# Performance work log

Hardware: AMD Instinct MI355X
Metric: run time of the kernel (lower is better)

The kernel has to match this reference:

```python
import jax, jax.numpy as jnp
import numpy as np

B, S, H = 8, 2048, 1024

def setup_inputs() -> dict:
    key = jax.random.key(0)
    k1, k2 = jax.random.split(key)
    inputs = jax.random.normal(k1, (B, S, H), dtype=jnp.float32)
    # PyTorch Linear weight [out, in]; init ~ U(-1/sqrt(H), 1/sqrt(H)) approximated with scaled normal
    W = jax.random.normal(k2, (H, H), dtype=jnp.float32) * (1.0 / np.sqrt(H))
    b = jnp.zeros((H,), dtype=jnp.float32)
    return {"inputs": inputs, "W": W, "b": b}

def reference(inputs, W, b):
    # QW = inputs @ W^T + b   (nn.Linear)
    QW = jnp.einsum('bsh,oh->bso', inputs, W) + b  # [B,S,H]
    # score = QW @ inputs^T  (no scaling, no mask)
    score = jnp.einsum('bqh,bkh->bqk', QW, inputs)  # [B,S,S]
    attn = jax.nn.softmax(score, axis=2)
    # output = attn @ inputs
    output = jnp.einsum('bqk,bkh->bqh', attn, inputs)  # [B,S,H]
    return output
```

## Files before the change

### kernel.cpp

```cpp
#include <hip/hip_runtime.h>
#include <hip/hip_bf16.h>
#include <hip/hip_fp16.h>

typedef unsigned short u16;
typedef __attribute__((ext_vector_type(8))) _Float16 f16x8;
typedef __attribute__((ext_vector_type(4))) float f32x4;

#define B_ 8
#define S_ 2048
#define H_ 1024
#define M_ (B_ * S_)

__device__ __forceinline__ u16 f2h(float f) {
  _Float16 h = (_Float16)f;
  return __builtin_bit_cast(u16, h);
}

__global__ void f32_to_f16_kernel(const float* __restrict__ x,
                                  u16* __restrict__ o, int n4) {
  int stride = gridDim.x * blockDim.x;
  for (int i = blockIdx.x * blockDim.x + threadIdx.x; i < n4; i += stride) {
    float4 v = reinterpret_cast<const float4*>(x)[i];
    ushort4 h;
    h.x = f2h(v.x); h.y = f2h(v.y); h.z = f2h(v.z); h.w = f2h(v.w);
    reinterpret_cast<ushort4*>(o)[i] = h;
  }
}

__global__ __launch_bounds__(256) void transpose_f32_kernel(
    const float* __restrict__ x, u16* __restrict__ xt, u16* __restrict__ xf) {
  __shared__ u16 t[64][72];
  int b = blockIdx.z, s0 = blockIdx.x * 64, h0 = blockIdx.y * 64;
  int tid = threadIdx.x;
  int row = tid & 63, seg = tid >> 6;
  const float* src = x + ((size_t)(b * S_ + s0 + row)) * H_ + h0 + seg * 16;
  u16* dstf = xf + ((size_t)(b * S_ + s0 + row)) * H_ + h0 + seg * 16;
#pragma unroll
  for (int j = 0; j < 4; ++j) {
    float4 v = reinterpret_cast<const float4*>(src)[j];
    ushort4 h;
    h.x = f2h(v.x); h.y = f2h(v.y); h.z = f2h(v.z); h.w = f2h(v.w);
    reinterpret_cast<ushort4*>(dstf)[j] = h;
    *reinterpret_cast<ushort4*>(&t[row][seg * 16 + j * 4]) = h;
  }
  __syncthreads();
  int hh = tid & 63, ss = tid >> 6;
  u16* dst = xt + ((size_t)(b * H_ + h0 + hh)) * S_ + s0 + ss * 16;
#pragma unroll
  for (int j = 0; j < 4; ++j) {
    ushort4 o;
    o.x = t[ss * 16 + j * 4 + 0][hh];
    o.y = t[ss * 16 + j * 4 + 1][hh];
    o.z = t[ss * 16 + j * 4 + 2][hh];
    o.w = t[ss * 16 + j * 4 + 3][hh];
    reinterpret_cast<ushort4*>(dst)[j] = o;
  }
}

__device__ __forceinline__ void async_stage16(const u16* g, u16* l) {
  __builtin_amdgcn_global_load_lds(
      (__attribute__((address_space(1))) void*)g,
      (__attribute__((address_space(3))) void*)l, 16, 0, 0);
}

template <int OM>
__global__ __launch_bounds__(512) void gemm8_kernel(
    const u16* __restrict__ A, const u16* __restrict__ B,
    float* __restrict__ Cf, u16* __restrict__ Ch,
    const float* __restrict__ bias,
    int lda, int ldb, int ldc, int K,
    long sAz, long sBz, long sCz) {
  __shared__ __align__(16) u16 sA[2][256 * 64];
  __shared__ __align__(16) u16 sB[2][256 * 64];

  int gx = gridDim.x, gy = gridDim.y;
  int nwg = gx * gy * gridDim.z;
  int wgid = blockIdx.x + gx * (blockIdx.y + gy * blockIdx.z);
  int q = nwg >> 3, r = nwg & 7;
  int xcd = wgid & 7, idx = wgid >> 3;
  int nid = (xcd < r ? xcd * (q + 1) : r * (q + 1) + (xcd - r) * q) + idx;
  int bxi = nid % gx, t2 = nid / gx;
  int byi = t2 % gy, bzi = t2 / gy;

  int tid = threadIdx.x, wave = tid >> 6, lane = tid & 63;
  int wm = wave >> 2, wn = wave & 3;
  int bm = bxi * 256, bn = byi * 256;
  long zA = (long)bzi * sAz;
  long zB = (long)bzi * sBz;
  long zC = (long)bzi * sCz;
  const u16* gA = A + zA + (size_t)bm * lda;
  const u16* gB = B + zB + (size_t)bn * ldb;

  int srow = tid >> 3;
  int scolb = (tid & 7) << 4;
  int sco = (scolb ^ ((srow & 7) << 4)) >> 1;
  size_t aO0 = (size_t)srow * lda + sco, aO1 = aO0 + (size_t)64 * lda;
  size_t bO0 = (size_t)srow * ldb + sco, bO1 = bO0 + (size_t)64 * ldb;
  int ld0 = srow * 64 + (scolb >> 1), ld1 = ld0 + 64 * 64;

  auto stgA = [&](int slot, int half, int kofs) {
    const u16* g = gA + (size_t)(half * 128) * lda + kofs;
    u16* l = &sA[slot][half * 8192];
    async_stage16(g + aO0, l + ld0);
    async_stage16(g + aO1, l + ld1);
  };
  auto stgB = [&](int slot, int half, int kofs) {
    const u16* g = gB + (size_t)(half * 128) * ldb + kofs;
    u16* l = &sB[slot][half * 8192];
    async_stage16(g + bO0, l + ld0);
    async_stage16(g + bO1, l + ld1);
  };

  int la = lane & 15;
  int kg = (lane >> 4) << 4;
  auto frag = [&](const u16* base, int row, int colb) -> f16x8 {
    int off = (row << 7) + (colb ^ ((row & 7) << 4));
    return *reinterpret_cast<const f16x8*>(
        reinterpret_cast<const char*>(base) + off);
  };

  f16x8 aF[4][2];
  f16x8 bF[2][2][2];
  f32x4 acc[8][4] = {};

  auto RA = [&](int slot, int qm) {
#pragma unroll
    for (int j = 0; j < 4; ++j)
#pragma unroll
      for (int ks = 0; ks < 2; ++ks)
        aF[j][ks] = frag(sA[slot], qm * 128 + (j * 2 + wm) * 16 + la,
                         ks * 64 + kg);
  };
  auto RB = [&](int slot, int qn) {
#pragma unroll
    for (int i = 0; i < 2; ++i)
#pragma unroll
      for (int ks = 0; ks < 2; ++ks)
        bF[qn][i][ks] = frag(sB[slot], qn * 128 + (i * 4 + wn) * 16 + la,
                             ks * 64 + kg);
  };
  auto MM = [&](int qm, int qn) {
#pragma unroll
    for (int ks = 0; ks < 2; ++ks)
#pragma unroll
      for (int j = 0; j < 4; ++j)
#pragma unroll
        for (int i = 0; i < 2; ++i)
          acc[qm * 4 + j][qn * 2 + i] = __builtin_amdgcn_mfma_f32_16x16x32_f16(
              aF[j][ks], bF[qn][i][ks], acc[qm * 4 + j][qn * 2 + i], 0, 0, 0);
  };

#define VM6 asm volatile("s_waitcnt vmcnt(6)" ::: "memory")
#define VM0 asm volatile("s_waitcnt vmcnt(0)" ::: "memory")
#define BAR __builtin_amdgcn_s_barrier()
#define LG0                                              \
  asm volatile("s_waitcnt lgkmcnt(0)" ::: "memory");     \
  __builtin_amdgcn_sched_barrier(0)
#define MFMA_CL(qm, qn)                 \
  __builtin_amdgcn_s_setprio(1);        \
  MM(qm, qn);                           \
  __builtin_amdgcn_s_setprio(0)

  int NT = K >> 6;
  stgA(0, 0, 0); stgB(0, 0, 0); stgB(0, 1, 0); stgA(0, 1, 0);
  if (NT > 1) { stgA(1, 0, 64); stgB(1, 1, 64); stgA(1, 1, 64); }
  VM6;
  BAR;

  for (int t = 0; t < NT; ++t) {
    int s = t & 1, ns = s ^ 1;
    int k1 = (t + 1) << 6, k2 = (t + 2) << 6;
    bool p1 = (t + 1 < NT), p2 = (t + 2 < NT);
    RA(s, 0); RB(s, 0);
    if (p1) stgB(ns, 0, k1);
    LG0; MFMA_CL(0, 0); BAR;
    RB(s, 1);
    if (p2) stgA(s, 0, k2);
    LG0; MFMA_CL(0, 1); BAR;
    RA(s, 1);
    if (p2) stgB(s, 1, k2);
    LG0; MFMA_CL(1, 1); BAR;
    if (p2) stgA(s, 1, k2);
    MFMA_CL(1, 0);
    if (t < NT - 2) { VM6; } else if (t == NT - 2) { VM0; }
    BAR;
  }
#undef VM6
#undef VM0
#undef BAR
#undef LG0
#undef MFMA_CL

#pragma unroll
  for (int mf = 0; mf < 8; ++mf) {
    int qm = mf >> 2, j = mf & 3;
    int row = bm + qm * 128 + (j * 2 + wm) * 16 + (lane >> 4) * 4;
#pragma unroll
    for (int nf = 0; nf < 4; ++nf) {
      int qn = nf >> 1, i = nf & 1;
      int col = bn + qn * 128 + (i * 4 + wn) * 16 + la;
#pragma unroll
      for (int r = 0; r < 4; ++r) {
        float v = acc[mf][nf][r];
        if constexpr (OM == 1) {
          Ch[zC + (size_t)(row + r) * ldc + col] = f2h(v + bias[col]);
        } else {
          Cf[zC + (size_t)(row + r) * ldc + col] = v;
        }
      }
    }
  }
}

__global__ __launch_bounds__(256) void softmax_kernel(const float* __restrict__ sc,
                                                      u16* __restrict__ attn,
                                                      int opitch) {
  __shared__ float red[4];
  size_t row = blockIdx.x;
  const float* p = sc + row * S_;
  u16* o = attn + row * (size_t)opitch;
  int t = threadIdx.x;
  float4 v0 = reinterpret_cast<const float4*>(p)[t];
  float4 v1 = reinterpret_cast<const float4*>(p)[t + 256];
  float mx = fmaxf(fmaxf(fmaxf(v0.x, v0.y), fmaxf(v0.z, v0.w)),
                   fmaxf(fmaxf(v1.x, v1.y), fmaxf(v1.z, v1.w)));
#pragma unroll
  for (int d = 32; d > 0; d >>= 1) mx = fmaxf(mx, __shfl_xor(mx, d));
  if ((t & 63) == 0) red[t >> 6] = mx;
  __syncthreads();
  mx = fmaxf(fmaxf(red[0], red[1]), fmaxf(red[2], red[3]));
  float e[8];
  e[0] = __expf(v0.x - mx); e[1] = __expf(v0.y - mx);
  e[2] = __expf(v0.z - mx); e[3] = __expf(v0.w - mx);
  e[4] = __expf(v1.x - mx); e[5] = __expf(v1.y - mx);
  e[6] = __expf(v1.z - mx); e[7] = __expf(v1.w - mx);
  float s = ((e[0] + e[1]) + (e[2] + e[3])) + ((e[4] + e[5]) + (e[6] + e[7]));
#pragma unroll
  for (int d = 32; d > 0; d >>= 1) s += __shfl_xor(s, d);
  __syncthreads();
  if ((t & 63) == 0) red[t >> 6] = s;
  __syncthreads();
  s = (red[0] + red[1]) + (red[2] + red[3]);
  float inv = 1.0f / s;
  ushort4 h0, h1;
  h0.x = f2h(e[0] * inv); h0.y = f2h(e[1] * inv);
  h0.z = f2h(e[2] * inv); h0.w = f2h(e[3] * inv);
  h1.x = f2h(e[4] * inv); h1.y = f2h(e[5] * inv);
  h1.z = f2h(e[6] * inv); h1.w = f2h(e[7] * inv);
  reinterpret_cast<ushort4*>(o)[t] = h0;
  reinterpret_cast<ushort4*>(o)[t + 256] = h1;
}

extern "C" void kernel_launch(void* const* d_in, const int* in_sizes, int n_in,
                              void* d_out, int out_size, void* d_ws, size_t ws_size,
                              hipStream_t stream) {
  const float* X = (const float*)d_in[0];
  const float* W = (const float*)d_in[1];
  const float* bias = (const float*)d_in[2];
  float* out = (float*)d_out;
  char* ws = (char*)d_ws;

  const size_t MB = 1ull << 20;
  u16* XF = (u16*)(ws);
  u16* WF = (u16*)(ws + 32 * MB);
  u16* XT = (u16*)(ws + 34 * MB);
  u16* QW = (u16*)(ws + 66 * MB);
  float* SC = (float*)(ws + 98 * MB);
  u16* PF = (u16*)(ws + 162 * MB);

  int plan = (ws_size >= 226 * MB) ? 2 : (ws_size >= 163 * MB) ? 1 : 0;
  int CB = (plan >= 1) ? 4 : 2;
  int nch = B_ / CB;

  f32_to_f16_kernel<<<1024, 256, 0, stream>>>(W, WF, H_ * H_ / 4);
  transpose_f32_kernel<<<dim3(S_ / 64, H_ / 64, B_), 256, 0, stream>>>(
      X, XT, XF);
  gemm8_kernel<1><<<dim3(M_ / 256, H_ / 256, 1), 512, 0, stream>>>(
      XF, WF, nullptr, QW, bias, H_, H_, H_, H_, 0, 0, 0);
  for (int ch = 0; ch < nch; ++ch) {
    long off = (long)ch * CB;
    gemm8_kernel<0><<<dim3(S_ / 256, S_ / 256, CB), 512, 0, stream>>>(
        QW + off * S_ * H_, XF + off * S_ * H_, SC, nullptr, nullptr,
        H_, H_, S_, H_, (long)S_ * H_, (long)S_ * H_, (long)S_ * S_);
    if (plan == 2) {
      softmax_kernel<<<CB * S_, 256, 0, stream>>>(
          SC, PF + off * S_ * S_, S_);
    } else {
      softmax_kernel<<<CB * S_, 256, 0, stream>>>(
          SC, (u16*)SC, 2 * S_);
      gemm8_kernel<0><<<dim3(S_ / 256, H_ / 256, CB), 512, 0, stream>>>(
          (u16*)SC, XT + off * (long)H_ * S_,
          out + off * (long)S_ * H_, nullptr, nullptr,
          2 * S_, S_, H_, S_, (long)S_ * 2 * S_, (long)H_ * S_, (long)S_ * H_);
    }
  }
  if (plan == 2) {
    gemm8_kernel<0><<<dim3(S_ / 256, H_ / 256, B_), 512, 0, stream>>>(
        PF, XT, out, nullptr, nullptr,
        S_, S_, H_, S_, (long)S_ * S_, (long)H_ * S_, (long)S_ * H_);
  }
}
```

Measured before the change: 263.7 us.

## Switch GEMM to 32x32x16 MFMA and always softmax in place

Replaces the 16x16x32 MFMA tiling with 32x32x16 MFMA instructions. Each wave now holds 4x2 accumulator tiles of 16 floats, with fragment loads and the epilogue row mapping rewritten to match. The host plan no longer writes fp16 probabilities to a separate buffer; softmax writes in place into the score buffer, and with enough workspace all 8 batches run as one chunk. The larger MFMA shape cuts LDS fragment reads per FLOP, while the scattered epilogue stores and larger chunk's scratch footprint may change memory behaviour.

Measured after the change: 274.5 us. +4.1%, slower.

```diff
diff --git a/kernel.cpp b/kernel.cpp
--- a/kernel.cpp
+++ b/kernel.cpp
@@ -4,7 +4,7 @@
 
 typedef unsigned short u16;
 typedef __attribute__((ext_vector_type(8))) _Float16 f16x8;
-typedef __attribute__((ext_vector_type(4))) float f32x4;
+typedef __attribute__((ext_vector_type(16))) float f32x16;
 
 #define B_ 8
 #define S_ 2048
@@ -111,43 +111,38 @@
     async_stage16(g + bO1, l + ld1);
   };
 
-  int la = lane & 15;
-  int kg = (lane >> 4) << 4;
+  int l31 = lane & 31;
+  int kg32 = (lane >> 5) << 4;
   auto frag = [&](const u16* base, int row, int colb) -> f16x8 {
     int off = (row << 7) + (colb ^ ((row & 7) << 4));
     return *reinterpret_cast<const f16x8*>(
         reinterpret_cast<const char*>(base) + off);
   };
 
-  f16x8 aF[4][2];
-  f16x8 bF[2][2][2];
-  f32x4 acc[8][4] = {};
+  f16x8 aF[2][4];
+  f16x8 bF[2][4];
+  f32x16 acc[4][2] = {};
 
   auto RA = [&](int slot, int qm) {
 #pragma unroll
-    for (int j = 0; j < 4; ++j)
-#pragma unroll
-      for (int ks = 0; ks < 2; ++ks)
-        aF[j][ks] = frag(sA[slot], qm * 128 + (j * 2 + wm) * 16 + la,
-                         ks * 64 + kg);
+    for (int mt = 0; mt < 2; ++mt)
+#pragma unroll
+      for (int ks = 0; ks < 4; ++ks)
+        aF[mt][ks] = frag(sA[slot], qm * 128 + wm * 64 + mt * 32 + l31,
+                          ks * 32 + kg32);
   };
   auto RB = [&](int slot, int qn) {
 #pragma unroll
-    for (int i = 0; i < 2; ++i)
-#pragma unroll
-      for (int ks = 0; ks < 2; ++ks)
-        bF[qn][i][ks] = frag(sB[slot], qn * 128 + (i * 4 + wn) * 16 + la,
-                             ks * 64 + kg);
+    for (int ks = 0; ks < 4; ++ks)
+      bF[qn][ks] = frag(sB[slot], qn * 128 + wn * 32 + l31, ks * 32 + kg32);
   };
   auto MM = [&](int qm, int qn) {
 #pragma unroll
-    for (int ks = 0; ks < 2; ++ks)
-#pragma unroll
-      for (int j = 0; j < 4; ++j)
-#pragma unroll
-        for (int i = 0; i < 2; ++i)
-          acc[qm * 4 + j][qn * 2 + i] = __builtin_amdgcn_mfma_f32_16x16x32_f16(
-              aF[j][ks], bF[qn][i][ks], acc[qm * 4 + j][qn * 2 + i], 0, 0, 0);
+    for (int ks = 0; ks < 4; ++ks)
+#pragma unroll
+      for (int mt = 0; mt < 2; ++mt)
+        acc[qm * 2 + mt][qn] = __builtin_amdgcn_mfma_f32_32x32x16_f16(
+            aF[mt][ks], bF[qn][ks], acc[qm * 2 + mt][qn], 0, 0, 0);
   };
 
 #define VM6 asm volatile("s_waitcnt vmcnt(6)" ::: "memory")
@@ -191,21 +186,22 @@
 #undef LG0
 #undef MFMA_CL
 
-#pragma unroll
-  for (int mf = 0; mf < 8; ++mf) {
-    int qm = mf >> 2, j = mf & 3;
-    int row = bm + qm * 128 + (j * 2 + wm) * 16 + (lane >> 4) * 4;
-#pragma unroll
-    for (int nf = 0; nf < 4; ++nf) {
-      int qn = nf >> 1, i = nf & 1;
-      int col = bn + qn * 128 + (i * 4 + wn) * 16 + la;
-#pragma unroll
-      for (int r = 0; r < 4; ++r) {
-        float v = acc[mf][nf][r];
+  int rsub = 4 * (lane >> 5);
+#pragma unroll
+  for (int mi = 0; mi < 4; ++mi) {
+    int qm = mi >> 1, mt = mi & 1;
+    int rowb = bm + qm * 128 + wm * 64 + mt * 32 + rsub;
+#pragma unroll
+    for (int ni = 0; ni < 2; ++ni) {
+      int col = bn + ni * 128 + wn * 32 + l31;
+#pragma unroll
+      for (int reg = 0; reg < 16; ++reg) {
+        int row = rowb + (reg & 3) + 8 * (reg >> 2);
+        float v = acc[mi][ni][reg];
         if constexpr (OM == 1) {
-          Ch[zC + (size_t)(row + r) * ldc + col] = f2h(v + bias[col]);
+          Ch[zC + (size_t)row * ldc + col] = f2h(v + bias[col]);
         } else {
-          Cf[zC + (size_t)(row + r) * ldc + col] = v;
+          Cf[zC + (size_t)row * ldc + col] = v;
         }
       }
     }
@@ -266,10 +262,8 @@
   u16* XT = (u16*)(ws + 34 * MB);
   u16* QW = (u16*)(ws + 66 * MB);
   float* SC = (float*)(ws + 98 * MB);
-  u16* PF = (u16*)(ws + 162 * MB);
-
-  int plan = (ws_size >= 226 * MB) ? 2 : (ws_size >= 163 * MB) ? 1 : 0;
-  int CB = (plan >= 1) ? 4 : 2;
+
+  int CB = (ws_size >= 226 * MB) ? 8 : 4;
   int nch = B_ / CB;
 
   f32_to_f16_kernel<<<1024, 256, 0, stream>>>(W, WF, H_ * H_ / 4);
@@ -282,21 +276,10 @@
     gemm8_kernel<0><<<dim3(S_ / 256, S_ / 256, CB), 512, 0, stream>>>(
         QW + off * S_ * H_, XF + off * S_ * H_, SC, nullptr, nullptr,
         H_, H_, S_, H_, (long)S_ * H_, (long)S_ * H_, (long)S_ * S_);
-    if (plan == 2) {
-      softmax_kernel<<<CB * S_, 256, 0, stream>>>(
-          SC, PF + off * S_ * S_, S_);
-    } else {
-      softmax_kernel<<<CB * S_, 256, 0, stream>>>(
-          SC, (u16*)SC, 2 * S_);
-      gemm8_kernel<0><<<dim3(S_ / 256, H_ / 256, CB), 512, 0, stream>>>(
-          (u16*)SC, XT + off * (long)H_ * S_,
-          out + off * (long)S_ * H_, nullptr, nullptr,
-          2 * S_, S_, H_, S_, (long)S_ * 2 * S_, (long)H_ * S_, (long)S_ * H_);
-    }
-  }
-  if (plan == 2) {
-    gemm8_kernel<0><<<dim3(S_ / 256, H_ / 256, B_), 512, 0, stream>>>(
-        PF, XT, out, nullptr, nullptr,
-        S_, S_, H_, S_, (long)S_ * S_, (long)H_ * S_, (long)S_ * H_);
-  }
-}
+    softmax_kernel<<<CB * S_, 256, 0, stream>>>(SC, (u16*)SC, 2 * S_);
+    gemm8_kernel<0><<<dim3(S_ / 256, H_ / 256, CB), 512, 0, stream>>>(
+        (u16*)SC, XT + off * (long)H_ * S_,
+        out + off * (long)S_ * H_, nullptr, nullptr,
+        2 * S_, S_, H_, S_, (long)S_ * 2 * S_, (long)H_ * S_, (long)S_ * H_);
+  }
+}
```

## Double-buffer MFMA fragments in GEMM and batch full attention chunks in place

Applied to the files above, without the earlier changes.

The GEMM inner loop now keeps separate register sets for the two A and two B quadrant fragments. It loads B for both quadrants up front and loads A1 while the first MFMA clusters run. The explicit lgkmcnt(0) waits and sched_barriers are dropped so LDS reads can overlap with MFMAs, at the cost of more VGPR pressure and relying on the compiler to insert the needed waits. The host plan also drops the separate PF probability buffer. It processes all 8 batches in one chunk (or 4 with less workspace), with softmax written in place and the P·V GEMM run per chunk.

New measurement: 257.5 us. -2.3%, faster.

```diff
diff --git a/kernel.cpp b/kernel.cpp
--- a/kernel.cpp
+++ b/kernel.cpp
@@ -119,27 +119,27 @@
         reinterpret_cast<const char*>(base) + off);
   };
 
-  f16x8 aF[4][2];
-  f16x8 bF[2][2][2];
+  f16x8 aF0[4][2], aF1[4][2];
+  f16x8 bF0[2][2], bF1[2][2];
   f32x4 acc[8][4] = {};
 
-  auto RA = [&](int slot, int qm) {
+  auto RA = [&](int slot, int qm, f16x8(&dst)[4][2]) {
 #pragma unroll
     for (int j = 0; j < 4; ++j)
 #pragma unroll
       for (int ks = 0; ks < 2; ++ks)
-        aF[j][ks] = frag(sA[slot], qm * 128 + (j * 2 + wm) * 16 + la,
-                         ks * 64 + kg);
-  };
-  auto RB = [&](int slot, int qn) {
+        dst[j][ks] = frag(sA[slot], qm * 128 + (j * 2 + wm) * 16 + la,
+                          ks * 64 + kg);
+  };
+  auto RB = [&](int slot, int qn, f16x8(&dst)[2][2]) {
 #pragma unroll
     for (int i = 0; i < 2; ++i)
 #pragma unroll
       for (int ks = 0; ks < 2; ++ks)
-        bF[qn][i][ks] = frag(sB[slot], qn * 128 + (i * 4 + wn) * 16 + la,
-                             ks * 64 + kg);
-  };
-  auto MM = [&](int qm, int qn) {
+        dst[i][ks] = frag(sB[slot], qn * 128 + (i * 4 + wn) * 16 + la,
+                          ks * 64 + kg);
+  };
+  auto MM = [&](int qm, int qn, f16x8(&a)[4][2], f16x8(&b)[2][2]) {
 #pragma unroll
     for (int ks = 0; ks < 2; ++ks)
 #pragma unroll
@@ -147,19 +147,14 @@
 #pragma unroll
         for (int i = 0; i < 2; ++i)
           acc[qm * 4 + j][qn * 2 + i] = __builtin_amdgcn_mfma_f32_16x16x32_f16(
-              aF[j][ks], bF[qn][i][ks], acc[qm * 4 + j][qn * 2 + i], 0, 0, 0);
+              a[j][ks], b[i][ks], acc[qm * 4 + j][qn * 2 + i], 0, 0, 0);
   };
 
 #define VM6 asm volatile("s_waitcnt vmcnt(6)" ::: "memory")
 #define VM0 asm volatile("s_waitcnt vmcnt(0)" ::: "memory")
 #define BAR __builtin_amdgcn_s_barrier()
-#define LG0                                              \
-  asm volatile("s_waitcnt lgkmcnt(0)" ::: "memory");     \
-  __builtin_amdgcn_sched_barrier(0)
-#define MFMA_CL(qm, qn)                 \
-  __builtin_amdgcn_s_setprio(1);        \
-  MM(qm, qn);                           \
-  __builtin_amdgcn_s_setprio(0)
+#define PRIO1 __builtin_amdgcn_s_setprio(1)
+#define PRIO0 __builtin_amdgcn_s_setprio(0)
 
   int NT = K >> 6;
   stgA(0, 0, 0); stgB(0, 0, 0); stgB(0, 1, 0); stgA(0, 1, 0);
@@ -171,25 +166,25 @@
     int s = t & 1, ns = s ^ 1;
     int k1 = (t + 1) << 6, k2 = (t + 2) << 6;
     bool p1 = (t + 1 < NT), p2 = (t + 2 < NT);
-    RA(s, 0); RB(s, 0);
+    RA(s, 0, aF0); RB(s, 0, bF0);
+    RB(s, 1, bF1);
     if (p1) stgB(ns, 0, k1);
-    LG0; MFMA_CL(0, 0); BAR;
-    RB(s, 1);
+    PRIO1; MM(0, 0, aF0, bF0); PRIO0; BAR;
+    RA(s, 1, aF1);
     if (p2) stgA(s, 0, k2);
-    LG0; MFMA_CL(0, 1); BAR;
-    RA(s, 1);
+    PRIO1; MM(0, 1, aF0, bF1); PRIO0; BAR;
     if (p2) stgB(s, 1, k2);
-    LG0; MFMA_CL(1, 1); BAR;
+    PRIO1; MM(1, 1, aF1, bF1); PRIO0; BAR;
     if (p2) stgA(s, 1, k2);
-    MFMA_CL(1, 0);
+    PRIO1; MM(1, 0, aF1, bF0); PRIO0;
     if (t < NT - 2) { VM6; } else if (t == NT - 2) { VM0; }
     BAR;
   }
 #undef VM6
 #undef VM0
 #undef BAR
-#undef LG0
-#undef MFMA_CL
+#undef PRIO1
+#undef PRIO0
 
 #pragma unroll
   for (int mf = 0; mf < 8; ++mf) {
@@ -266,10 +261,8 @@
   u16* XT = (u16*)(ws + 34 * MB);
   u16* QW = (u16*)(ws + 66 * MB);
   float* SC = (float*)(ws + 98 * MB);
-  u16* PF = (u16*)(ws + 162 * MB);
-
-  int plan = (ws_size >= 226 * MB) ? 2 : (ws_size >= 163 * MB) ? 1 : 0;
-  int CB = (plan >= 1) ? 4 : 2;
+
+  int CB = (ws_size >= 226 * MB) ? 8 : 4;
   int nch = B_ / CB;
 
   f32_to_f16_kernel<<<1024, 256, 0, stream>>>(W, WF, H_ * H_ / 4);
@@ -282,21 +275,10 @@
     gemm8_kernel<0><<<dim3(S_ / 256, S_ / 256, CB), 512, 0, stream>>>(
         QW + off * S_ * H_, XF + off * S_ * H_, SC, nullptr, nullptr,
         H_, H_, S_, H_, (long)S_ * H_, (long)S_ * H_, (long)S_ * S_);
-    if (plan == 2) {
-      softmax_kernel<<<CB * S_, 256, 0, stream>>>(
-          SC, PF + off * S_ * S_, S_);
-    } else {
-      softmax_kernel<<<CB * S_, 256, 0, stream>>>(
-          SC, (u16*)SC, 2 * S_);
-      gemm8_kernel<0><<<dim3(S_ / 256, H_ / 256, CB), 512, 0, stream>>>(
-          (u16*)SC, XT + off * (long)H_ * S_,
-          out + off * (long)S_ * H_, nullptr, nullptr,
-          2 * S_, S_, H_, S_, (long)S_ * 2 * S_, (long)H_ * S_, (long)S_ * H_);
-    }
-  }
-  if (plan == 2) {
-    gemm8_kernel<0><<<dim3(S_ / 256, H_ / 256, B_), 512, 0, stream>>>(
-        PF, XT, out, nullptr, nullptr,
-        S_, S_, H_, S_, (long)S_ * S_, (long)H_ * S_, (long)S_ * H_);
-  }
-}
+    softmax_kernel<<<CB * S_, 256, 0, stream>>>(SC, (u16*)SC, 2 * S_);
+    gemm8_kernel<0><<<dim3(S_ / 256, H_ / 256, CB), 512, 0, stream>>>(
+        (u16*)SC, XT + off * (long)H_ * S_,
+        out + off * (long)S_ * H_, nullptr, nullptr,
+        2 * S_, S_, H_, S_, (long)S_ * 2 * S_, (long)H_ * S_, (long)S_ * H_);
+  }
+}
```
